# Kernel optimization log

Hardware: AMD Instinct MI355X
Metric: run time of the kernel (lower is better)

The kernel has to match this reference:

```python
import math
import jax, jax.numpy as jnp
import numpy as np

N_HEADS = 2


def _scatter_softmax(scores, seg, num_segments):
    # softmax over edges grouped by destination (head) node, per attention head
    m = jax.ops.segment_max(scores, seg, num_segments=num_segments)  # [N, H]
    e = jnp.exp(scores - m[seg])
    s = jax.ops.segment_sum(e, seg, num_segments=num_segments)  # [N, H]
    return e / s[seg]


def _l2norm(x, eps=1e-12):
    # torch F.normalize(dim=1)
    n = jnp.sqrt(jnp.sum(x * x, axis=1, keepdims=True))
    return x / jnp.maximum(n, eps)


def setup_inputs() -> dict:
    key = jax.random.key(0)
    ks = jax.random.split(key, 8)
    dims, n_relations = 128, 10
    n_users, n_entities = 30000, 60000
    n_edges, n_inter = 600000, 800000
    user_emb = jax.random.normal(ks[0], (n_users, dims), dtype=jnp.float32)
    entity_emb = jax.random.normal(ks[1], (n_entities, dims), dtype=jnp.float32)
    inter_edge = jnp.stack([
        jax.random.randint(ks[2], (n_inter,), 0, n_users),
        jax.random.randint(ks[3], (n_inter,), 0, n_entities),
    ], axis=0)
    inter_edge_w = jax.random.uniform(ks[4], (n_inter,), dtype=jnp.float32)
    edge_index = jax.random.randint(ks[5], (2, n_edges), 0, n_entities)
    edge_type = jax.random.randint(ks[6], (n_edges,), 1, n_relations + 1)  # 1-based
    relation_emb = 0.1 * jax.random.normal(ks[7], (n_relations, dims), dtype=jnp.float32)
    W_Q = 0.1 * jax.random.normal(jax.random.fold_in(key, 99), (dims, dims), dtype=jnp.float32)
    return {"layers_num": 2, "user_emb": user_emb, "entity_emb": entity_emb,
            "inter_edge": inter_edge, "inter_edge_w": inter_edge_w,
            "edge_index": edge_index, "edge_type": edge_type,
            "relation_emb": relation_emb, "W_Q": W_Q}


def reference(layers_num, user_emb, entity_emb, inter_edge, inter_edge_w,
              edge_index, edge_type, relation_emb, W_Q):
    dims = entity_emb.shape[1]
    d_k = dims // N_HEADS
    n_entities = entity_emb.shape[0]
    n_users = user_emb.shape[0]
    head, tail = edge_index[0], edge_index[1]
    rel = relation_emb[edge_type - 1]  # [E, D]
    rel_h = rel.reshape(-1, N_HEADS, d_k)
    u_idx, i_idx = inter_edge[0], inter_edge[1]

    def agg_layer(u_emb, e_emb):
        head_emb = e_emb[head]                                   # [E, D]
        tail_emb = e_emb[tail]                                   # [E, D]
        q = (head_emb @ W_Q).reshape(-1, N_HEADS, d_k)
        k = (tail_emb @ W_Q).reshape(-1, N_HEADS, d_k) * rel_h
        score = jnp.sum(q * k, axis=-1) / math.sqrt(d_k)          # [E, H]
        attn = _scatter_softmax(score, head, n_entities)          # [E, H]
        value = (tail_emb * rel).reshape(-1, N_HEADS, d_k)
        weighted = (value * attn[..., None]).reshape(-1, dims)
        entity_agg = jax.ops.segment_sum(weighted, head, num_segments=n_entities)
        entity_agg = _l2norm(entity_agg)
        item_agg = inter_edge_w[:, None] * e_emb[i_idx]           # [Ei, D]
        user_agg = jax.ops.segment_sum(item_agg, u_idx, num_segments=n_users)
        return entity_agg, user_agg

    user_embs = [user_emb]
    entity_embs = [entity_emb]
    for _ in range(layers_num):
        entity_emb, user_emb = agg_layer(user_emb, entity_emb)
        user_embs.append(user_emb)
        entity_embs.append(entity_emb)
    user_out = jnp.mean(jnp.stack(user_embs, axis=1), axis=1)
    entity_out = jnp.mean(jnp.stack(entity_embs, axis=1), axis=1)
    return (user_out, entity_out)
```

## Files before the change

kernel.cpp:

```cpp
#include <hip/hip_runtime.h>
#include <hip/hip_bf16.h>

#define D 128
typedef unsigned short u16;
typedef unsigned int u32;

__device__ __forceinline__ float bf2f(u16 u) {
    return __uint_as_float(((u32)u) << 16);
}
__device__ __forceinline__ u16 f2bf(float f) {
    union { float f; u32 u; } a; a.f = f;
    u32 r = (a.u + 0x7FFF + ((a.u >> 16) & 1)) >> 16;
    return (u16)r;
}
__device__ __forceinline__ float2 bf2x2(u32 v) {
    float2 r;
    r.x = __uint_as_float(v << 16);
    r.y = __uint_as_float(v & 0xFFFF0000u);
    return r;
}
__device__ __forceinline__ u32 packbf2(float a, float b) {
    return (u32)f2bf(a) | ((u32)f2bf(b) << 16);
}
__device__ __forceinline__ float ldIn(const void* p, size_t i, int isBf) {
    return isBf ? bf2f(((const u16*)p)[i]) : ((const float*)p)[i];
}
__device__ __forceinline__ void stOut(void* p, size_t i, float v, int isBf) {
    if (isBf) ((u16*)p)[i] = f2bf(v);
    else      ((float*)p)[i] = v;
}

__global__ void sniff_k(const u16* __restrict__ probe, int* __restrict__ flag) {
    int t = threadIdx.x;
    u16 v = probe[2 * t];
    int ex = (v >> 7) & 0xFF;
    int sane = (ex == 0) || (ex >= 0x70 && ex <= 0x8A);
    unsigned long long m = __ballot(sane != 0);
    if (t == 0) *flag = (__popcll(m) >= 48) ? 1 : 0;
}

__global__ void convert_k(const void* __restrict__ src, u16* __restrict__ dst,
                          int n, const int* __restrict__ flagp) {
    int i = blockIdx.x * blockDim.x + threadIdx.x;
    int isBf = *flagp;
    if (i < n) dst[i] = isBf ? ((const u16*)src)[i] : f2bf(((const float*)src)[i]);
}

__global__ void zero_k(int* __restrict__ p, int n) {
    int i = blockIdx.x * blockDim.x + threadIdx.x;
    if (i < n) p[i] = 0;
}
__global__ void hist_k(const int* __restrict__ keys, int n, int nDst,
                       int* __restrict__ cntP1) {
    int i = blockIdx.x * blockDim.x + threadIdx.x;
    if (i < n) {
        int k = min(max(keys[i], 0), nDst - 1);
        atomicAdd(&cntP1[k + 1], 1);
    }
}
__global__ void copy_k(const int* __restrict__ src, int* __restrict__ dst, int n) {
    int i = blockIdx.x * blockDim.x + threadIdx.x;
    if (i < n) dst[i] = src[i];
}
__global__ void scatter_e(const int* __restrict__ head, const int* __restrict__ tail,
                          const int* __restrict__ etyp, int n, int nDst, int nEnt,
                          int* __restrict__ pos, int* __restrict__ pack) {
    int i = blockIdx.x * blockDim.x + threadIdx.x;
    if (i < n) {
        int k = min(max(head[i], 0), nDst - 1);
        int p = atomicAdd(&pos[k], 1);
        if (p >= 0 && p < n) {
            int tl = min(max(tail[i], 0), nEnt - 1);
            int rt = min(max(etyp[i] - 1, 0), 9);
            pack[p] = tl | (rt << 24);
        }
    }
}
__global__ void scatter_u(const int* __restrict__ u_idx, const int* __restrict__ i_idx,
                          const void* __restrict__ iw, int n, int nDst, int nEnt,
                          int* __restrict__ pos, int* __restrict__ item,
                          float* __restrict__ wt, const int* __restrict__ flagp) {
    int i = blockIdx.x * blockDim.x + threadIdx.x;
    int isBf = *flagp;
    if (i < n) {
        int k = min(max(u_idx[i], 0), nDst - 1);
        int p = atomicAdd(&pos[k], 1);
        if (p >= 0 && p < n) {
            item[p] = min(max(i_idx[i], 0), nEnt - 1);
            wt[p] = ldIn(iw, i, isBf);
        }
    }
}

__global__ __launch_bounds__(256) void block_sum_k(const int* __restrict__ buf, int n,
                                                   int* __restrict__ bsum) {
    __shared__ int waveTot[4];
    int b = blockIdx.x, t = threadIdx.x, lane = t & 63, wave = t >> 6;
    int idx = 1 + b * 1024 + t * 4;
    int s = 0;
    #pragma unroll
    for (int k = 0; k < 4; ++k)
        if (idx + k <= n) s += buf[idx + k];
    #pragma unroll
    for (int o = 32; o > 0; o >>= 1) s += __shfl_xor(s, o);
    if (lane == 0) waveTot[wave] = s;
    __syncthreads();
    if (t == 0) bsum[b] = waveTot[0] + waveTot[1] + waveTot[2] + waveTot[3];
}
__global__ void scan_bsums_k(int* __restrict__ bsum, int nb) {
    int t = threadIdx.x;
    int v = (t < nb) ? bsum[t] : 0;
    int x = v;
    #pragma unroll
    for (int o = 1; o < 64; o <<= 1) {
        int y = __shfl_up(x, o);
        if (t >= o) x += y;
    }
    if (t < nb) bsum[t] = x - v;
}
__global__ __launch_bounds__(256) void block_scan_k(int* __restrict__ buf, int n,
                                                    const int* __restrict__ bsum) {
    __shared__ int waveTot[4];
    int b = blockIdx.x, t = threadIdx.x, lane = t & 63, wave = t >> 6;
    int idx = 1 + b * 1024 + t * 4;
    int v0 = 0, v1 = 0, v2 = 0, v3 = 0;
    if (idx     <= n) v0 = buf[idx];
    if (idx + 1 <= n) v1 = buf[idx + 1];
    if (idx + 2 <= n) v2 = buf[idx + 2];
    if (idx + 3 <= n) v3 = buf[idx + 3];
    int s = v0 + v1 + v2 + v3;
    int x = s;
    #pragma unroll
    for (int o = 1; o < 64; o <<= 1) {
        int y = __shfl_up(x, o);
        if (lane >= o) x += y;
    }
    if (lane == 63) waveTot[wave] = x;
    __syncthreads();
    int off = bsum[b];
    for (int wv = 0; wv < wave; ++wv) off += waveTot[wv];
    int r0 = off + (x - s) + v0;
    int r1 = r0 + v1;
    int r2 = r1 + v2;
    int r3 = r2 + v3;
    if (idx     <= n) buf[idx]     = r0;
    if (idx + 1 <= n) buf[idx + 1] = r1;
    if (idx + 2 <= n) buf[idx + 2] = r2;
    if (idx + 3 <= n) buf[idx + 3] = r3;
}

#define GEMM_ROWS 64
#define WT_STRIDE 136
typedef __attribute__((ext_vector_type(8))) short bf16x8;
typedef __attribute__((ext_vector_type(4))) float f32x4;

__global__ __launch_bounds__(256) void gemm_P3(const u16* __restrict__ E,
                                               const u16* __restrict__ WQ,
                                               u16* __restrict__ P, int nRows) {
    __shared__ u16 sWT[D * WT_STRIDE];
    int t = threadIdx.x;
    for (int i = t; i < D * D; i += 256) {
        int k = i >> 7, c = i & 127;
        sWT[c * WT_STRIDE + k] = WQ[i];
    }
    __syncthreads();
    int wave = t >> 6, lane = t & 63;
    int m = lane & 15, quad = lane >> 4;
    int row0 = blockIdx.x * GEMM_ROWS + wave * 16;
    int rowA = min(row0 + m, nRows - 1);
    const u16* erow = E + (size_t)rowA * D;
    bf16x8 afrag[4];
    #pragma unroll
    for (int ks = 0; ks < 4; ++ks)
        afrag[ks] = *(const bf16x8*)(erow + ks * 32 + quad * 8);
    #pragma unroll
    for (int ct = 0; ct < 8; ++ct) {
        f32x4 acc = {0.f, 0.f, 0.f, 0.f};
        const u16* wcol = sWT + (ct * 16 + m) * WT_STRIDE + quad * 8;
        #pragma unroll
        for (int ks = 0; ks < 4; ++ks) {
            bf16x8 bfrag = *(const bf16x8*)(wcol + ks * 32);
            acc = __builtin_amdgcn_mfma_f32_16x16x32_bf16(afrag[ks], bfrag, acc, 0, 0, 0);
        }
        #pragma unroll
        for (int reg = 0; reg < 4; ++reg) {
            int r = row0 + quad * 4 + reg;
            if (r < nRows) P[(size_t)r * D + ct * 16 + m] = f2bf(acc[reg]);
        }
    }
}

__global__ __launch_bounds__(256) void entity_agg3(
    const u16* __restrict__ P, const u16* __restrict__ eCur,
    const u16* __restrict__ relb, const int* __restrict__ e_off,
    const int* __restrict__ e_pack, void* __restrict__ eOut,
    const u32* __restrict__ e0b, int finalMode, size_t outElemOff,
    int nEnt, const int* __restrict__ flagp) {
    __shared__ u16 sRel[10 * D];
    int tid = threadIdx.x;
    for (int i = tid; i < 10 * D; i += 256) sRel[i] = relb[i];
    __syncthreads();
    int wid = (blockIdx.x * blockDim.x + tid) >> 6;
    int lane = tid & 63;
    if (wid >= nEnt) return;
    const u32* P32 = (const u32*)P;
    const u32* E32 = (const u32*)eCur;
    const u32* R32 = (const u32*)sRel;
    float2 q = bf2x2(P32[(size_t)wid * 64 + lane]);
    const float SC = 0.125f * 1.44269504f;
    float l = 0.f, a0 = 0.f, a1 = 0.f;
    int s = e_off[wid], e = e_off[wid + 1];
    for (int j0 = s; j0 < e; j0 += 64) {
        int B = min(64, e - j0);
        int pk = (lane < B) ? e_pack[j0 + lane] : 0;
        int pv = __shfl(pk, 0);
        size_t off = (size_t)(pv & 0xFFFFFF) * 64 + lane;
        u32 ptv = P32[off];
        u32 evv = E32[off];
        for (int i = 0; i < B; ++i) {
            u32 cpt = ptv, cev = evv;
            int cpv = pv;
            if (i + 1 < B) {
                pv = __shfl(pk, i + 1);
                off = (size_t)(pv & 0xFFFFFF) * 64 + lane;
                ptv = P32[off];
                evv = E32[off];
            }
            int rt = (int)((u32)cpv >> 24);
            float2 rr = bf2x2(R32[rt * 64 + lane]);
            float2 pt = bf2x2(cpt);
            float2 ev = bf2x2(cev);
            float v0 = ev.x * rr.x;
            float v1 = ev.y * rr.y;
            float prod = q.x * pt.x * rr.x + q.y * pt.y * rr.y;
            #pragma unroll
            for (int o = 16; o > 0; o >>= 1) prod += __shfl_xor(prod, o);
            float p = exp2f(prod * SC);
            l += p;
            a0 = fmaf(p, v0, a0);
            a1 = fmaf(p, v1, a1);
        }
    }
    float o0 = (l > 0.f) ? a0 / l : 0.f;
    float o1 = (l > 0.f) ? a1 / l : 0.f;
    float ss = o0 * o0 + o1 * o1;
    #pragma unroll
    for (int o = 32; o > 0; o >>= 1) ss += __shfl_xor(ss, o);
    float inv = 1.f / fmaxf(sqrtf(ss), 1e-12f);
    float w0 = o0 * inv, w1 = o1 * inv;
    size_t b32i = (size_t)wid * 64 + lane;
    if (finalMode) {
        int isBf = *flagp;
        const float k = 1.0f / 3.0f;
        size_t be = 2 * b32i;
        float2 ec = bf2x2(E32[b32i]);
        float2 e0 = bf2x2(e0b[b32i]);
        w0 = (e0.x + ec.x + w0) * k;
        w1 = (e0.y + ec.y + w1) * k;
        stOut(eOut, outElemOff + be, w0, isBf);
        stOut(eOut, outElemOff + be + 1, w1, isBf);
    } else {
        ((u32*)eOut)[b32i] = packbf2(w0, w1);
    }
}

__global__ __launch_bounds__(256) void user_agg3(
    const u16* __restrict__ eCur, const int* __restrict__ u_off,
    const int* __restrict__ u_item, const float* __restrict__ u_wt,
    float* __restrict__ usum, const void* __restrict__ ueRaw,
    void* __restrict__ outU, int finalMode, int nU, int nEnt,
    const int* __restrict__ flagp) {
    int wid = (blockIdx.x * blockDim.x + threadIdx.x) >> 6;
    int lane = threadIdx.x & 63;
    if (wid >= nU) return;
    const u32* E32 = (const u32*)eCur;
    float a0 = 0.f, a1 = 0.f;
    int s = u_off[wid], e = u_off[wid + 1];
    for (int j0 = s; j0 < e; j0 += 64) {
        int B = min(64, e - j0);
        int it = (lane < B) ? u_item[j0 + lane] : 0;
        float wv = (lane < B) ? u_wt[j0 + lane] : 0.f;
        int i0 = __shfl(it, 0);
        u32 ev0 = E32[(size_t)i0 * 64 + lane];
        u32 ev1 = 0;
        if (B > 1) {
            int i1 = __shfl(it, 1);
            ev1 = E32[(size_t)i1 * 64 + lane];
        }
        for (int i = 0; i < B; ++i) {
            u32 cur = ev0;
            ev0 = ev1;
            if (i + 2 < B) {
                int nx = __shfl(it, i + 2);
                ev1 = E32[(size_t)nx * 64 + lane];
            }
            float wc = __shfl(wv, i);
            float2 f = bf2x2(cur);
            a0 = fmaf(wc, f.x, a0);
            a1 = fmaf(wc, f.y, a1);
        }
    }
    size_t b32i = (size_t)wid * 64 + lane;
    if (finalMode) {
        int isBf = *flagp;
        const float k = 1.0f / 3.0f;
        size_t be = 2 * b32i;
        float2 us = ((const float2*)usum)[b32i];
        stOut(outU, be, (ldIn(ueRaw, be, isBf) + us.x + a0) * k, isBf);
        stOut(outU, be + 1, (ldIn(ueRaw, be + 1, isBf) + us.y + a1) * k, isBf);
    } else {
        ((float2*)usum)[b32i] = make_float2(a0, a1);
    }
}

extern "C" void kernel_launch(void* const* d_in, const int* in_sizes, int n_in,
                              void* d_out, int out_size, void* d_ws, size_t ws_size,
                              hipStream_t stream) {
    const void* ue  = d_in[1];
    const void* ee  = d_in[2];
    const int*  itr = (const int*)d_in[3];
    const void* iw  = d_in[4];
    const int*  eix = (const int*)d_in[5];
    const int*  ety = (const int*)d_in[6];
    const void* rel = d_in[7];
    const void* wq  = d_in[8];

    const int nU = in_sizes[1] / D;
    const int nE = in_sizes[2] / D;
    const int Ei = in_sizes[4];
    const int Ee = in_sizes[6];
    const int nRel = in_sizes[7] / D;

    const int* u_idx = itr;
    const int* i_idx = itr + Ei;
    const int* head  = eix;
    const int* tail  = eix + Ee;

    char* w = (char*)d_ws;
    auto alloc = [&](size_t bytes) {
        char* p = w;
        w += (bytes + 255) & ~(size_t)255;
        return p;
    };
    int*   flag  = (int*)alloc(256);
    int*  e_off  = (int*)alloc((size_t)(nE + 1) * 4);
    int*  u_off  = (int*)alloc((size_t)(nU + 1) * 4);
    int*  e_pos  = (int*)alloc((size_t)nE * 4);
    int*  u_pos  = (int*)alloc((size_t)nU * 4);
    int*  e_pack = (int*)alloc((size_t)Ee * 4);
    int*  u_item = (int*)alloc((size_t)Ei * 4);
    float* u_wt  = (float*)alloc((size_t)Ei * 4);
    int*  bsumE  = (int*)alloc(64 * 4);
    int*  bsumU  = (int*)alloc(64 * 4);
    u16*  eeb    = (u16*)alloc((size_t)nE * D * 2);
    u16*  wqb    = (u16*)alloc((size_t)D * D * 2);
    u16*  relb   = (u16*)alloc((size_t)nRel * D * 2);
    u16*  eL1    = (u16*)alloc((size_t)nE * D * 2);
    u16*  P      = (u16*)alloc((size_t)nE * D * 2);
    float* usum  = (float*)alloc((size_t)nU * D * 4);

    if ((size_t)(w - (char*)d_ws) > ws_size) {
        return;
    }

    sniff_k<<<1, 64, 0, stream>>>((const u16*)ue, flag);

    convert_k<<<(nE * D + 255) / 256, 256, 0, stream>>>(ee, eeb, nE * D, flag);
    convert_k<<<(D * D + 255) / 256, 256, 0, stream>>>(wq, wqb, D * D, flag);
    convert_k<<<(nRel * D + 255) / 256, 256, 0, stream>>>(rel, relb, nRel * D, flag);

    const int nbE = (nE + 1023) / 1024;
    const int nbU = (nU + 1023) / 1024;
    zero_k<<<(nE + 1 + 255) / 256, 256, 0, stream>>>(e_off, nE + 1);
    zero_k<<<(nU + 1 + 255) / 256, 256, 0, stream>>>(u_off, nU + 1);
    hist_k<<<(Ee + 255) / 256, 256, 0, stream>>>(head, Ee, nE, e_off);
    hist_k<<<(Ei + 255) / 256, 256, 0, stream>>>(u_idx, Ei, nU, u_off);
    block_sum_k<<<nbE, 256, 0, stream>>>(e_off, nE, bsumE);
    block_sum_k<<<nbU, 256, 0, stream>>>(u_off, nU, bsumU);
    scan_bsums_k<<<1, 64, 0, stream>>>(bsumE, nbE);
    scan_bsums_k<<<1, 64, 0, stream>>>(bsumU, nbU);
    block_scan_k<<<nbE, 256, 0, stream>>>(e_off, nE, bsumE);
    block_scan_k<<<nbU, 256, 0, stream>>>(u_off, nU, bsumU);
    copy_k<<<(nE + 255) / 256, 256, 0, stream>>>(e_off, e_pos, nE);
    copy_k<<<(nU + 255) / 256, 256, 0, stream>>>(u_off, u_pos, nU);
    scatter_e<<<(Ee + 255) / 256, 256, 0, stream>>>(head, tail, ety, Ee, nE, nE,
                                                    e_pos, e_pack);
    scatter_u<<<(Ei + 255) / 256, 256, 0, stream>>>(u_idx, i_idx, iw, Ei, nU, nE,
                                                    u_pos, u_item, u_wt, flag);

    const int entBlocks  = (nE * 64 + 255) / 256;
    const int userBlocks = (nU * 64 + 255) / 256;
    const int gemmBlocks = (nE + GEMM_ROWS - 1) / GEMM_ROWS;

    gemm_P3<<<gemmBlocks, 256, 0, stream>>>(eeb, wqb, P, nE);
    entity_agg3<<<entBlocks, 256, 0, stream>>>(P, eeb, relb, e_off, e_pack,
                                               eL1, nullptr, 0, 0, nE, flag);
    user_agg3<<<userBlocks, 256, 0, stream>>>(eeb, u_off, u_item, u_wt,
                                              usum, nullptr, nullptr, 0, nU, nE, flag);

    gemm_P3<<<gemmBlocks, 256, 0, stream>>>(eL1, wqb, P, nE);
    entity_agg3<<<entBlocks, 256, 0, stream>>>(P, eL1, relb, e_off, e_pack,
                                               d_out, (const u32*)eeb, 1,
                                               (size_t)nU * D, nE, flag);
    user_agg3<<<userBlocks, 256, 0, stream>>>(eL1, u_off, u_item, u_wt,
                                              usum, ue, d_out, 1, nU, nE, flag);
}
```

Measured before the change: 564.9 us.

## Interleave projected and raw entity rows in fp16 for single-gather edge loop

Switches intermediate storage from bf16 to fp16 and interleaves the projected query/key row with the raw entity row into one 8-byte-per-lane buffer, so each edge in the attention loop issues one 64-bit gather instead of two 32-bit gathers. The key/value products use packed half math and a dot2 instruction. This adds an extra pack kernel and a scattered write pattern in the GEMM epilogue and conversion. fp16 range could in principle overflow where bf16 did not.

```diff
diff --git a/kernel.cpp b/kernel.cpp
--- a/kernel.cpp
+++ b/kernel.cpp
@@ -4,6 +4,9 @@
 #define D 128
 typedef unsigned short u16;
 typedef unsigned int u32;
+typedef _Float16 h2 __attribute__((ext_vector_type(2)));
+typedef _Float16 f16x8 __attribute__((ext_vector_type(8)));
+typedef float f32x4 __attribute__((ext_vector_type(4)));
 
 __device__ __forceinline__ float bf2f(u16 u) {
     return __uint_as_float(((u32)u) << 16);
@@ -13,14 +16,27 @@
     u32 r = (a.u + 0x7FFF + ((a.u >> 16) & 1)) >> 16;
     return (u16)r;
 }
-__device__ __forceinline__ float2 bf2x2(u32 v) {
-    float2 r;
-    r.x = __uint_as_float(v << 16);
-    r.y = __uint_as_float(v & 0xFFFF0000u);
-    return r;
-}
-__device__ __forceinline__ u32 packbf2(float a, float b) {
-    return (u32)f2bf(a) | ((u32)f2bf(b) << 16);
+__device__ __forceinline__ u16 f2h(float f) {
+    union { _Float16 h; u16 u; } c; c.h = (_Float16)f;
+    return c.u;
+}
+__device__ __forceinline__ h2 u2h2(u32 v) {
+    union { u32 u; h2 h; } c; c.u = v;
+    return c.h;
+}
+__device__ __forceinline__ u32 h22u(h2 h) {
+    union { u32 u; h2 h; } c; c.h = h;
+    return c.u;
+}
+__device__ __forceinline__ u32 packh2(float a, float b) {
+    return (u32)f2h(a) | ((u32)f2h(b) << 16);
+}
+__device__ __forceinline__ float hdot2(h2 a, h2 b, float c) {
+#if __has_builtin(__builtin_amdgcn_fdot2)
+    return __builtin_amdgcn_fdot2(a, b, c, false);
+#else
+    return (float)a.x * (float)b.x + (float)a.y * (float)b.y + c;
+#endif
 }
 __device__ __forceinline__ float ldIn(const void* p, size_t i, int isBf) {
     return isBf ? bf2f(((const u16*)p)[i]) : ((const float*)p)[i];
@@ -39,11 +55,26 @@
     if (t == 0) *flag = (__popcll(m) >= 48) ? 1 : 0;
 }
 
-__global__ void convert_k(const void* __restrict__ src, u16* __restrict__ dst,
-                          int n, const int* __restrict__ flagp) {
+__global__ void convert_h_k(const void* __restrict__ src, u16* __restrict__ dst,
+                            int n, const int* __restrict__ flagp) {
     int i = blockIdx.x * blockDim.x + threadIdx.x;
     int isBf = *flagp;
-    if (i < n) dst[i] = isBf ? ((const u16*)src)[i] : f2bf(((const float*)src)[i]);
+    if (i < n) dst[i] = f2h(ldIn(src, i, isBf));
+}
+__global__ void convert_e_k(const void* __restrict__ src, u16* __restrict__ eeb,
+                            u16* __restrict__ PE, int n, const int* __restrict__ flagp) {
+    int i = blockIdx.x * blockDim.x + threadIdx.x;
+    int isBf = *flagp;
+    if (i < n) {
+        u16 h = f2h(ldIn(src, i, isBf));
+        eeb[i] = h;
+        int ent = i >> 7, c = i & 127;
+        PE[(size_t)ent * 256 + ((c >> 1) << 2) + 2 + (c & 1)] = h;
+    }
+}
+__global__ void packE_k(const u32* __restrict__ eL1p, u32* __restrict__ PEu, int n64) {
+    int i = blockIdx.x * blockDim.x + threadIdx.x;
+    if (i < n64) PEu[(size_t)(i >> 6) * 128 + 2 * (i & 63) + 1] = eL1p[i];
 }
 
 __global__ void zero_k(int* __restrict__ p, int n) {
@@ -151,12 +182,9 @@
 
 #define GEMM_ROWS 64
 #define WT_STRIDE 136
-typedef __attribute__((ext_vector_type(8))) short bf16x8;
-typedef __attribute__((ext_vector_type(4))) float f32x4;
-
-__global__ __launch_bounds__(256) void gemm_P3(const u16* __restrict__ E,
+__global__ __launch_bounds__(256) void gemm_P4(const u16* __restrict__ E,
                                                const u16* __restrict__ WQ,
-                                               u16* __restrict__ P, int nRows) {
+                                               u16* __restrict__ PE, int nRows) {
     __shared__ u16 sWT[D * WT_STRIDE];
     int t = threadIdx.x;
     for (int i = t; i < D * D; i += 256) {
@@ -169,44 +197,45 @@
     int row0 = blockIdx.x * GEMM_ROWS + wave * 16;
     int rowA = min(row0 + m, nRows - 1);
     const u16* erow = E + (size_t)rowA * D;
-    bf16x8 afrag[4];
+    f16x8 afrag[4];
     #pragma unroll
     for (int ks = 0; ks < 4; ++ks)
-        afrag[ks] = *(const bf16x8*)(erow + ks * 32 + quad * 8);
+        afrag[ks] = *(const f16x8*)(erow + ks * 32 + quad * 8);
     #pragma unroll
     for (int ct = 0; ct < 8; ++ct) {
         f32x4 acc = {0.f, 0.f, 0.f, 0.f};
         const u16* wcol = sWT + (ct * 16 + m) * WT_STRIDE + quad * 8;
         #pragma unroll
         for (int ks = 0; ks < 4; ++ks) {
-            bf16x8 bfrag = *(const bf16x8*)(wcol + ks * 32);
-            acc = __builtin_amdgcn_mfma_f32_16x16x32_bf16(afrag[ks], bfrag, acc, 0, 0, 0);
-        }
+            f16x8 bfrag = *(const f16x8*)(wcol + ks * 32);
+            acc = __builtin_amdgcn_mfma_f32_16x16x32_f16(afrag[ks], bfrag, acc, 0, 0, 0);
+        }
+        int c = ct * 16 + m;
+        size_t pbase = ((size_t)(c >> 1) << 2) + (c & 1);
         #pragma unroll
         for (int reg = 0; reg < 4; ++reg) {
             int r = row0 + quad * 4 + reg;
-            if (r < nRows) P[(size_t)r * D + ct * 16 + m] = f2bf(acc[reg]);
-        }
-    }
-}
-
-__global__ __launch_bounds__(256) void entity_agg3(
-    const u16* __restrict__ P, const u16* __restrict__ eCur,
-    const u16* __restrict__ relb, const int* __restrict__ e_off,
-    const int* __restrict__ e_pack, void* __restrict__ eOut,
-    const u32* __restrict__ e0b, int finalMode, size_t outElemOff,
+            if (r < nRows) PE[(size_t)r * 256 + pbase] = f2h(acc[reg]);
+        }
+    }
+}
+
+__global__ __launch_bounds__(256) void entity_agg4(
+    const uint2* __restrict__ PE, const u16* __restrict__ relh,
+    const int* __restrict__ e_off, const int* __restrict__ e_pack,
+    u32* __restrict__ eL1p,
+    const u32* __restrict__ eebp,
+    void* __restrict__ outE, int finalMode, size_t outElemOff,
     int nEnt, const int* __restrict__ flagp) {
-    __shared__ u16 sRel[10 * D];
+    __shared__ u32 sRel[10 * 64];
     int tid = threadIdx.x;
-    for (int i = tid; i < 10 * D; i += 256) sRel[i] = relb[i];
+    for (int i = tid; i < 10 * 64; i += 256) sRel[i] = ((const u32*)relh)[i];
     __syncthreads();
     int wid = (blockIdx.x * blockDim.x + tid) >> 6;
     int lane = tid & 63;
     if (wid >= nEnt) return;
-    const u32* P32 = (const u32*)P;
-    const u32* E32 = (const u32*)eCur;
-    const u32* R32 = (const u32*)sRel;
-    float2 q = bf2x2(P32[(size_t)wid * 64 + lane]);
+    const u32* PEu = (const u32*)PE;
+    h2 q = u2h2(PEu[(size_t)wid * 128 + 2 * lane]);
     const float SC = 0.125f * 1.44269504f;
     float l = 0.f, a0 = 0.f, a1 = 0.f;
     int s = e_off[wid], e = e_off[wid + 1];
@@ -214,31 +243,27 @@
         int B = min(64, e - j0);
         int pk = (lane < B) ? e_pack[j0 + lane] : 0;
         int pv = __shfl(pk, 0);
-        size_t off = (size_t)(pv & 0xFFFFFF) * 64 + lane;
-        u32 ptv = P32[off];
-        u32 evv = E32[off];
+        uint2 pe = PE[(size_t)(pv & 0xFFFFFF) * 64 + lane];
         for (int i = 0; i < B; ++i) {
-            u32 cpt = ptv, cev = evv;
+            uint2 cpe = pe;
             int cpv = pv;
             if (i + 1 < B) {
                 pv = __shfl(pk, i + 1);
-                off = (size_t)(pv & 0xFFFFFF) * 64 + lane;
-                ptv = P32[off];
-                evv = E32[off];
+                pe = PE[(size_t)(pv & 0xFFFFFF) * 64 + lane];
             }
             int rt = (int)((u32)cpv >> 24);
-            float2 rr = bf2x2(R32[rt * 64 + lane]);
-            float2 pt = bf2x2(cpt);
-            float2 ev = bf2x2(cev);
-            float v0 = ev.x * rr.x;
-            float v1 = ev.y * rr.y;
-            float prod = q.x * pt.x * rr.x + q.y * pt.y * rr.y;
+            h2 rr = u2h2(sRel[rt * 64 + lane]);
+            h2 pt = u2h2(cpe.x);
+            h2 ev = u2h2(cpe.y);
+            h2 kq = pt * rr;
+            h2 v  = ev * rr;
+            float prod = hdot2(q, kq, 0.f);
             #pragma unroll
             for (int o = 16; o > 0; o >>= 1) prod += __shfl_xor(prod, o);
             float p = exp2f(prod * SC);
             l += p;
-            a0 = fmaf(p, v0, a0);
-            a1 = fmaf(p, v1, a1);
+            a0 = fmaf(p, (float)v.x, a0);
+            a1 = fmaf(p, (float)v.y, a1);
         }
     }
     float o0 = (l > 0.f) ? a0 / l : 0.f;
@@ -248,24 +273,24 @@
     for (int o = 32; o > 0; o >>= 1) ss += __shfl_xor(ss, o);
     float inv = 1.f / fmaxf(sqrtf(ss), 1e-12f);
     float w0 = o0 * inv, w1 = o1 * inv;
-    size_t b32i = (size_t)wid * 64 + lane;
+    size_t pri = (size_t)wid * 64 + lane;
     if (finalMode) {
         int isBf = *flagp;
         const float k = 1.0f / 3.0f;
-        size_t be = 2 * b32i;
-        float2 ec = bf2x2(E32[b32i]);
-        float2 e0 = bf2x2(e0b[b32i]);
-        w0 = (e0.x + ec.x + w0) * k;
-        w1 = (e0.y + ec.y + w1) * k;
-        stOut(eOut, outElemOff + be, w0, isBf);
-        stOut(eOut, outElemOff + be + 1, w1, isBf);
+        h2 ec = u2h2(PEu[(size_t)wid * 128 + 2 * lane + 1]);
+        h2 e0 = u2h2(eebp[pri]);
+        w0 = ((float)e0.x + (float)ec.x + w0) * k;
+        w1 = ((float)e0.y + (float)ec.y + w1) * k;
+        size_t be = outElemOff + (size_t)wid * D + 2 * lane;
+        stOut(outE, be, w0, isBf);
+        stOut(outE, be + 1, w1, isBf);
     } else {
-        ((u32*)eOut)[b32i] = packbf2(w0, w1);
-    }
-}
-
-__global__ __launch_bounds__(256) void user_agg3(
-    const u16* __restrict__ eCur, const int* __restrict__ u_off,
+        eL1p[pri] = packh2(w0, w1);
+    }
+}
+
+__global__ __launch_bounds__(256) void user_agg4(
+    const u32* __restrict__ eCurp, const int* __restrict__ u_off,
     const int* __restrict__ u_item, const float* __restrict__ u_wt,
     float* __restrict__ usum, const void* __restrict__ ueRaw,
     void* __restrict__ outU, int finalMode, int nU, int nEnt,
@@ -273,7 +298,6 @@
     int wid = (blockIdx.x * blockDim.x + threadIdx.x) >> 6;
     int lane = threadIdx.x & 63;
     if (wid >= nU) return;
-    const u32* E32 = (const u32*)eCur;
     float a0 = 0.f, a1 = 0.f;
     int s = u_off[wid], e = u_off[wid + 1];
     for (int j0 = s; j0 < e; j0 += 64) {
@@ -281,23 +305,23 @@
         int it = (lane < B) ? u_item[j0 + lane] : 0;
         float wv = (lane < B) ? u_wt[j0 + lane] : 0.f;
         int i0 = __shfl(it, 0);
-        u32 ev0 = E32[(size_t)i0 * 64 + lane];
+        u32 ev0 = eCurp[(size_t)i0 * 64 + lane];
         u32 ev1 = 0;
         if (B > 1) {
             int i1 = __shfl(it, 1);
-            ev1 = E32[(size_t)i1 * 64 + lane];
+            ev1 = eCurp[(size_t)i1 * 64 + lane];
         }
         for (int i = 0; i < B; ++i) {
             u32 cur = ev0;
             ev0 = ev1;
             if (i + 2 < B) {
                 int nx = __shfl(it, i + 2);
-                ev1 = E32[(size_t)nx * 64 + lane];
+                ev1 = eCurp[(size_t)nx * 64 + lane];
             }
             float wc = __shfl(wv, i);
-            float2 f = bf2x2(cur);
-            a0 = fmaf(wc, f.x, a0);
-            a1 = fmaf(wc, f.y, a1);
+            h2 f = u2h2(cur);
+            a0 = fmaf(wc, (float)f.x, a0);
+            a1 = fmaf(wc, (float)f.y, a1);
         }
     }
     size_t b32i = (size_t)wid * 64 + lane;
@@ -353,10 +377,10 @@
     int*  bsumE  = (int*)alloc(64 * 4);
     int*  bsumU  = (int*)alloc(64 * 4);
     u16*  eeb    = (u16*)alloc((size_t)nE * D * 2);
-    u16*  wqb    = (u16*)alloc((size_t)D * D * 2);
-    u16*  relb   = (u16*)alloc((size_t)nRel * D * 2);
+    u16*  wqh    = (u16*)alloc((size_t)D * D * 2);
+    u16*  relh   = (u16*)alloc((size_t)nRel * D * 2);
     u16*  eL1    = (u16*)alloc((size_t)nE * D * 2);
-    u16*  P      = (u16*)alloc((size_t)nE * D * 2);
+    u16*  PE     = (u16*)alloc((size_t)nE * D * 4);
     float* usum  = (float*)alloc((size_t)nU * D * 4);
 
     if ((size_t)(w - (char*)d_ws) > ws_size) {
@@ -365,9 +389,9 @@
 
     sniff_k<<<1, 64, 0, stream>>>((const u16*)ue, flag);
 
-    convert_k<<<(nE * D + 255) / 256, 256, 0, stream>>>(ee, eeb, nE * D, flag);
-    convert_k<<<(D * D + 255) / 256, 256, 0, stream>>>(wq, wqb, D * D, flag);
-    convert_k<<<(nRel * D + 255) / 256, 256, 0, stream>>>(rel, relb, nRel * D, flag);
+    convert_e_k<<<(nE * D + 255) / 256, 256, 0, stream>>>(ee, eeb, PE, nE * D, flag);
+    convert_h_k<<<(D * D + 255) / 256, 256, 0, stream>>>(wq, wqh, D * D, flag);
+    convert_h_k<<<(nRel * D + 255) / 256, 256, 0, stream>>>(rel, relh, nRel * D, flag);
 
     const int nbE = (nE + 1023) / 1024;
     const int nbU = (nU + 1023) / 1024;
@@ -392,16 +416,18 @@
     const int userBlocks = (nU * 64 + 255) / 256;
     const int gemmBlocks = (nE + GEMM_ROWS - 1) / GEMM_ROWS;
 
-    gemm_P3<<<gemmBlocks, 256, 0, stream>>>(eeb, wqb, P, nE);
-    entity_agg3<<<entBlocks, 256, 0, stream>>>(P, eeb, relb, e_off, e_pack,
-                                               eL1, nullptr, 0, 0, nE, flag);
-    user_agg3<<<userBlocks, 256, 0, stream>>>(eeb, u_off, u_item, u_wt,
+    gemm_P4<<<gemmBlocks, 256, 0, stream>>>(eeb, wqh, PE, nE);
+    entity_agg4<<<entBlocks, 256, 0, stream>>>((const uint2*)PE, relh, e_off, e_pack,
+                                               (u32*)eL1, nullptr, nullptr, 0, 0,
+                                               nE, flag);
+    user_agg4<<<userBlocks, 256, 0, stream>>>((const u32*)eeb, u_off, u_item, u_wt,
                                               usum, nullptr, nullptr, 0, nU, nE, flag);
 
-    gemm_P3<<<gemmBlocks, 256, 0, stream>>>(eL1, wqb, P, nE);
-    entity_agg3<<<entBlocks, 256, 0, stream>>>(P, eL1, relb, e_off, e_pack,
-                                               d_out, (const u32*)eeb, 1,
+    packE_k<<<(nE * 64 + 255) / 256, 256, 0, stream>>>((const u32*)eL1, (u32*)PE, nE * 64);
+    gemm_P4<<<gemmBlocks, 256, 0, stream>>>(eL1, wqh, PE, nE);
+    entity_agg4<<<entBlocks, 256, 0, stream>>>((const uint2*)PE, relh, e_off, e_pack,
+                                               nullptr, (const u32*)eeb, d_out, 1,
                                                (size_t)nU * D, nE, flag);
-    user_agg3<<<userBlocks, 256, 0, stream>>>(eL1, u_off, u_item, u_wt,
+    user_agg4<<<userBlocks, 256, 0, stream>>>((const u32*)eL1, u_off, u_item, u_wt,
                                               usum, ue, d_out, 1, nU, nE, flag);
 }
```

Result: slower. 612.4 us (+8.4%).
